# Performance work log

Hardware: AMD Instinct MI355X
Metric: run time of the kernel (lower is better)

## Reference

```python
import jax, jax.numpy as jnp
import numpy as np

B, D, E, H, OUT = 4096, 1024, 8, 4096, 1024


def setup_inputs() -> dict:
    key = jax.random.key(0)
    ks = jax.random.split(key, 8)
    s_in = 1.0 / np.sqrt(D)
    s_h = 1.0 / np.sqrt(H)
    return {
        "x": jax.random.normal(ks[0], (B, D), dtype=jnp.float32),
        "Wg": jax.random.uniform(ks[1], (D, E), minval=-s_in, maxval=s_in, dtype=jnp.float32),
        "bg": jnp.zeros((E,), dtype=jnp.float32),
        "W1": jax.random.uniform(ks[2], (E, D, H), minval=-s_in, maxval=s_in, dtype=jnp.float32),
        "b1": jnp.zeros((E, H), dtype=jnp.float32),
        "W2": jax.random.uniform(ks[3], (E, H, OUT), minval=-s_h, maxval=s_h, dtype=jnp.float32),
        "b2": jnp.zeros((E, OUT), dtype=jnp.float32),
        "w_bal": jnp.float32(0.01),
    }


def reference(x, Wg, bg, W1, b1, W2, b2, w_bal):
    # Gating: softmax then top-1 (== argmax of logits)
    gate_logits = x @ Wg + bg                      # [B, E]
    assign = jnp.argmax(gate_logits, axis=1)       # [B] top-1 expert
    onehot = jax.nn.one_hot(assign, E, dtype=x.dtype)  # [B, E] dispatch mask

    # Dense dispatch: run every expert MLP, combine by one-hot (top-1 select).
    # Original returns raw expert output (no gate-prob scaling).
    h = jax.nn.relu(jnp.einsum("bd,edh->ebh", x, W1) + b1[:, None, :])  # [E, B, H]
    y = jnp.einsum("ebh,eho->ebo", h, W2) + b2[:, None, :]              # [E, B, OUT]
    output = jnp.einsum("ebo,be->bo", y, onehot)                        # [B, OUT]

    # Load-balance loss on per-expert token counts
    loads = onehot.sum(axis=0)                     # [E]
    balance_loss = jnp.sum((loads - loads.mean()) ** 2) / E
    return output, balance_loss * w_bal
```

## Files before the change

kernel.cpp:

```cpp
#include <hip/hip_runtime.h>
#include <hip/hip_bf16.h>

typedef unsigned short u16;
typedef __attribute__((ext_vector_type(8))) short bf16x8;
typedef __attribute__((ext_vector_type(4))) float f32x4;

#define BTOK 4096
#define DDIM 1024
#define NEXP 8
#define HDIM 4096
#define ODIM 1024
#define MAXTILES 40
#define MAXROWS (MAXTILES * 128)

__device__ __forceinline__ u16 f2bf(float f) {
  unsigned u = __float_as_uint(f);
  return (u16)((u + 0x7FFFu + ((u >> 16) & 1u)) >> 16);
}
__device__ __forceinline__ u16 cvt_bf(float f) {
  __hip_bfloat16 h = __float2bfloat16(f);
  u16 r;
  __builtin_memcpy(&r, &h, 2);
  return r;
}

__device__ __forceinline__ void gload16(const void* g, void* l) {
  __builtin_amdgcn_global_load_lds(
      (const __attribute__((address_space(1))) void*)g,
      (__attribute__((address_space(3))) void*)l, 16, 0, 0);
}

__global__ __launch_bounds__(256) void init_kernel(int* __restrict__ ctrl,
                                                   int* __restrict__ rowmap) {
  int i = blockIdx.x * 256 + threadIdx.x;
  if (i < 1024)
    ctrl[i] = 0;
  else
    rowmap[i - 1024] = -1;
}

__global__ __launch_bounds__(256) void gate_kernel(
    const float* __restrict__ x, const float* __restrict__ Wg,
    const float* __restrict__ bg, int* __restrict__ assign,
    int* __restrict__ counts) {
  int wave = threadIdx.x >> 6;
  int lane = threadIdx.x & 63;
  int b = blockIdx.x * 4 + wave;
  const float* xr = x + (size_t)b * DDIM;
  double acc[NEXP];
#pragma unroll
  for (int e = 0; e < NEXP; ++e) acc[e] = 0.0;
  for (int d = lane; d < DDIM; d += 64) {
    float xv = xr[d];
    const float4* wrow = (const float4*)(Wg + d * NEXP);
    float4 w0 = wrow[0], w1 = wrow[1];
    acc[0] += (double)xv * (double)w0.x;
    acc[1] += (double)xv * (double)w0.y;
    acc[2] += (double)xv * (double)w0.z;
    acc[3] += (double)xv * (double)w0.w;
    acc[4] += (double)xv * (double)w1.x;
    acc[5] += (double)xv * (double)w1.y;
    acc[6] += (double)xv * (double)w1.z;
    acc[7] += (double)xv * (double)w1.w;
  }
#pragma unroll
  for (int e = 0; e < NEXP; ++e) {
    double v = acc[e];
#pragma unroll
    for (int off = 32; off > 0; off >>= 1) v += __shfl_xor(v, off);
    acc[e] = v;
  }
  if (lane == 0) {
    int best = 0;
    double bv = acc[0] + (double)bg[0];
#pragma unroll
    for (int e = 1; e < NEXP; ++e) {
      double v = acc[e] + (double)bg[e];
      if (v > bv) { bv = v; best = e; }
    }
    assign[b] = best;
    atomicAdd(&counts[best], 1);
  }
}

__global__ void setup_kernel(const int* __restrict__ counts,
                             const float* __restrict__ wbal,
                             int* __restrict__ offp, int* __restrict__ tile_e,
                             int* __restrict__ tile_m, int* __restrict__ meta,
                             float* __restrict__ loss_out) {
  if (threadIdx.x != 0 || blockIdx.x != 0) return;
  int off = 0, nt = 0;
  for (int e = 0; e < NEXP; ++e) {
    offp[e] = off;
    int pc = (counts[e] + 127) & ~127;
    for (int t = 0; t < (pc >> 7); ++t) {
      tile_e[nt] = e;
      tile_m[nt] = off + t * 128;
      ++nt;
    }
    off += pc;
  }
  offp[NEXP] = off;
  meta[0] = nt;
  float mean = (float)BTOK / (float)NEXP;
  float s = 0.f;
  for (int e = 0; e < NEXP; ++e) {
    float d = (float)counts[e] - mean;
    s += d * d;
  }
  loss_out[0] = s / (float)NEXP * wbal[0];
}

__global__ __launch_bounds__(256) void gather_kernel(
    const float* __restrict__ x, const int* __restrict__ assign,
    const int* __restrict__ offp, int* __restrict__ fill,
    int* __restrict__ rowmap, u16* __restrict__ xg) {
  int b = blockIdx.x;
  __shared__ int srow;
  if (threadIdx.x == 0) {
    int e = assign[b];
    int pos = atomicAdd(&fill[e], 1);
    int row = offp[e] + pos;
    rowmap[row] = b;
    srow = row;
  }
  __syncthreads();
  int row = srow;
  float4 v = *(const float4*)(x + (size_t)b * DDIM + threadIdx.x * 4);
  ushort4 o;
  o.x = f2bf(v.x);
  o.y = f2bf(v.y);
  o.z = f2bf(v.z);
  o.w = f2bf(v.w);
  *(ushort4*)(xg + (size_t)row * DDIM + threadIdx.x * 4) = o;
}

template <int MODE, int LDA, int LDN>
__global__ __launch_bounds__(256, 3) void moe_gemm(
    const u16* __restrict__ A, const float* __restrict__ W, size_t eStride,
    const float* __restrict__ bias, const int* __restrict__ tile_e,
    const int* __restrict__ tile_m, const int* __restrict__ meta,
    u16* __restrict__ Hout, float* __restrict__ P, size_t pStride, int nkt) {
  const int nx = gridDim.x;
  const int nwg = nx * gridDim.y;
  const int orig = blockIdx.y * nx + blockIdx.x;
  const int q = nwg >> 3;
  const int wg = (orig & 7) * q + (orig >> 3);
  const int bx = wg % nx, by = wg / nx;
  if (bx >= meta[0]) return;
  const int e = tile_e[bx];
  const int m0 = tile_m[bx];
  const int n0 = by * 128;
  const int kOff = blockIdx.z * nkt * 32;

  __shared__ __align__(16) u16 lds[2 * 8192];

  const int tid = threadIdx.x;
  const int lane = tid & 63;
  const int wave = tid >> 6;
  const int wr = wave >> 1, wc = wave & 1;
  const int fr = lane & 15;
  const int kqr = lane >> 4;

  const int r0 = tid >> 2, k0 = (tid & 3) ^ ((r0 >> 1) & 3);
  const int r1 = (tid + 256) >> 2, k1 = ((tid + 256) & 3) ^ ((r1 >> 1) & 3);
  const u16* aS0 = A + (size_t)(m0 + r0) * LDA + kOff + k0 * 8;
  const u16* aS1 = A + (size_t)(m0 + r1) * LDA + kOff + k1 * 8;
  const int dst0 = (tid & ~63) * 8;
  const int dst1 = dst0 + 2048;

  const int bc = tid & 127;
  const int bq0 = tid >> 7;
  const float* bRow = W + (size_t)e * eStride + (size_t)kOff * LDN + n0 + bc;
  const int bu0 = (bc * 4 + (bq0 ^ ((bc >> 1) & 3))) * 8;
  const int bu1 = (bc * 4 + ((bq0 + 2) ^ ((bc >> 1) & 3))) * 8;

  int aOff[4], bOff[4];
#pragma unroll
  for (int i = 0; i < 4; ++i) {
    int r = wr * 64 + i * 16 + fr;
    aOff[i] = (r * 4 + (kqr ^ ((r >> 1) & 3))) * 8;
    int c = wc * 64 + i * 16 + fr;
    bOff[i] = (c * 4 + (kqr ^ ((c >> 1) & 3))) * 8;
  }

  f32x4 acc[4][4];
#pragma unroll
  for (int i = 0; i < 4; ++i)
#pragma unroll
    for (int j = 0; j < 4; ++j)
#pragma unroll
      for (int r = 0; r < 4; ++r) acc[i][j][r] = 0.f;

  float fb[16];
  auto loadB = [&](int kt) {
    const float* p = bRow + (size_t)kt * 32 * LDN;
#pragma unroll
    for (int i = 0; i < 8; ++i) fb[i] = p[(size_t)(bq0 * 8 + i) * LDN];
#pragma unroll
    for (int i = 0; i < 8; ++i) fb[8 + i] = p[(size_t)((bq0 + 2) * 8 + i) * LDN];
  };
  auto writeB = [&](int c) {
    u16* ldsB = lds + c * 8192 + 4096;
    alignas(16) u16 tA[8], tB[8];
#pragma unroll
    for (int i = 0; i < 8; ++i) tA[i] = cvt_bf(fb[i]);
#pragma unroll
    for (int i = 0; i < 8; ++i) tB[i] = cvt_bf(fb[8 + i]);
    *(bf16x8*)&ldsB[bu0] = *(const bf16x8*)tA;
    *(bf16x8*)&ldsB[bu1] = *(const bf16x8*)tB;
  };
  auto stageA = [&](int c, int kt) {
    const int ko = kt * 32;
    u16* base = lds + c * 8192;
    gload16(aS0 + ko, base + dst0);
    gload16(aS1 + ko, base + dst1);
  };
  auto compute = [&](int c) {
    const u16* base = lds + c * 8192;
    bf16x8 af[4], bfr[4];
#pragma unroll
    for (int i = 0; i < 4; ++i) {
      af[i] = *(const bf16x8*)(base + aOff[i]);
      bfr[i] = *(const bf16x8*)(base + 4096 + bOff[i]);
    }
#pragma unroll
    for (int i = 0; i < 4; ++i)
#pragma unroll
      for (int j = 0; j < 4; ++j)
        acc[i][j] = __builtin_amdgcn_mfma_f32_16x16x32_bf16(af[i], bfr[j],
                                                            acc[i][j], 0, 0, 0);
  };

  loadB(0);
  stageA(0, 0);
  writeB(0);
  __syncthreads();
  int cur = 0;
#pragma unroll 1
  for (int kt = 0; kt < nkt - 1; ++kt) {
    loadB(kt + 1);
    stageA(cur ^ 1, kt + 1);
    compute(cur);
    writeB(cur ^ 1);
    __syncthreads();
    cur ^= 1;
  }
  compute(cur);

  if constexpr (MODE == 0) {
#pragma unroll
    for (int i = 0; i < 4; ++i) {
      int rbase = m0 + wr * 64 + i * 16 + (lane >> 4) * 4;
#pragma unroll
      for (int j = 0; j < 4; ++j) {
        int col = n0 + wc * 64 + j * 16 + fr;
        float bv = bias[e * LDN + col];
#pragma unroll
        for (int r = 0; r < 4; ++r) {
          float v = acc[i][j][r] + bv;
          v = v > 0.f ? v : 0.f;
          Hout[(size_t)(rbase + r) * LDN + col] = f2bf(v);
        }
      }
    }
  } else {
    float* Pp = P + blockIdx.z * pStride;
#pragma unroll
    for (int i = 0; i < 4; ++i) {
      int rbase = m0 + wr * 64 + i * 16 + (lane >> 4) * 4;
#pragma unroll
      for (int j = 0; j < 4; ++j) {
        int col = n0 + wc * 64 + j * 16 + fr;
#pragma unroll
        for (int r = 0; r < 4; ++r)
          Pp[(size_t)(rbase + r) * ODIM + col] = acc[i][j][r];
      }
    }
  }
}

__global__ __launch_bounds__(256) void reduce_kernel(
    const float* __restrict__ P, size_t pStride, const int* __restrict__ rowmap,
    const int* __restrict__ tile_e, const int* __restrict__ tile_m,
    const int* __restrict__ meta, const float* __restrict__ b2,
    float* __restrict__ out) {
  if ((int)blockIdx.x >= meta[0]) return;
  const int e = tile_e[blockIdx.x];
  const int m0 = tile_m[blockIdx.x];
  const int c0 = blockIdx.y * 128;
#pragma unroll 1
  for (int it = 0; it < 16; ++it) {
    int idx = it * 256 + threadIdx.x;
    int r = idx >> 5, cq = idx & 31;
    int row = m0 + r;
    int tok = rowmap[row];
    if (tok < 0) continue;
    int c = c0 + cq * 4;
    float4 a = *(const float4*)(P + (size_t)row * ODIM + c);
    float4 b = *(const float4*)(P + pStride + (size_t)row * ODIM + c);
    float4 bb = *(const float4*)(b2 + (size_t)e * ODIM + c);
    float4 o;
    o.x = a.x + b.x + bb.x;
    o.y = a.y + b.y + bb.y;
    o.z = a.z + b.z + bb.z;
    o.w = a.w + b.w + bb.w;
    *(float4*)(out + (size_t)tok * ODIM + c) = o;
  }
}

extern "C" void kernel_launch(void* const* d_in, const int* in_sizes, int n_in,
                              void* d_out, int out_size, void* d_ws,
                              size_t ws_size, hipStream_t stream) {
  const float* x = (const float*)d_in[0];
  const float* Wg = (const float*)d_in[1];
  const float* bg = (const float*)d_in[2];
  const float* W1 = (const float*)d_in[3];
  const float* b1 = (const float*)d_in[4];
  const float* W2 = (const float*)d_in[5];
  const float* b2 = (const float*)d_in[6];
  const float* wbal = (const float*)d_in[7];
  float* out = (float*)d_out;

  char* ws = (char*)d_ws;
  int* counts = (int*)(ws + 0);
  int* fill = (int*)(ws + 64);
  int* offp = (int*)(ws + 128);
  int* meta = (int*)(ws + 192);
  int* tile_e = (int*)(ws + 256);
  int* tile_m = (int*)(ws + 512);
  int* assign = (int*)(ws + 4096);
  int* rowmap = (int*)(ws + 20480);
  u16* xg = (u16*)(ws + 65536);
  u16* h = (u16*)(ws + 10551296);
  float* P = (float*)(ws + 52494336);
  const size_t pStride = (size_t)MAXROWS * ODIM;

  init_kernel<<<24, 256, 0, stream>>>((int*)ws, rowmap);
  gate_kernel<<<BTOK / 4, 256, 0, stream>>>(x, Wg, bg, assign, counts);
  setup_kernel<<<1, 64, 0, stream>>>(counts, wbal, offp, tile_e, tile_m, meta,
                                     out + (size_t)BTOK * ODIM);
  gather_kernel<<<BTOK, 256, 0, stream>>>(x, assign, offp, fill, rowmap, xg);

  moe_gemm<0, DDIM, HDIM><<<dim3(MAXTILES, HDIM / 128, 1), 256, 0, stream>>>(
      xg, W1, (size_t)DDIM * HDIM, b1, tile_e, tile_m, meta, h, nullptr, 0,
      DDIM / 32);
  moe_gemm<1, HDIM, ODIM><<<dim3(MAXTILES, ODIM / 128, 2), 256, 0, stream>>>(
      h, W2, (size_t)HDIM * ODIM, nullptr, tile_e, tile_m, meta, nullptr, P,
      pStride, HDIM / 64);

  reduce_kernel<<<dim3(MAXTILES, ODIM / 128), 256, 0, stream>>>(
      P, pStride, rowmap, tile_e, tile_m, meta, b2, out);
}
```

Before: 327.8 us.

## Deepen MoE GEMM pipeline with triple-buffered A and two-ahead B prefetch

```diff
diff --git a/kernel.cpp b/kernel.cpp
--- a/kernel.cpp
+++ b/kernel.cpp
@@ -153,7 +153,8 @@
   const int n0 = by * 128;
   const int kOff = blockIdx.z * nkt * 32;
 
-  __shared__ __align__(16) u16 lds[2 * 8192];
+  __shared__ __align__(16) u16 Alds[3 * 4096];
+  __shared__ __align__(16) u16 Blds[2 * 4096];
 
   const int tid = threadIdx.x;
   const int lane = tid & 63;
@@ -192,37 +193,39 @@
 #pragma unroll
       for (int r = 0; r < 4; ++r) acc[i][j][r] = 0.f;
 
-  float fb[16];
-  auto loadB = [&](int kt) {
+  float fb0[16], fb1[16];
+
+  auto stageA = [&](int buf, int kt) {
+    const int ko = kt * 32;
+    u16* base = Alds + buf * 4096;
+    gload16(aS0 + ko, base + dst0);
+    gload16(aS1 + ko, base + dst1);
+  };
+  auto loadB = [&](float (&f)[16], int kt) {
     const float* p = bRow + (size_t)kt * 32 * LDN;
 #pragma unroll
-    for (int i = 0; i < 8; ++i) fb[i] = p[(size_t)(bq0 * 8 + i) * LDN];
-#pragma unroll
-    for (int i = 0; i < 8; ++i) fb[8 + i] = p[(size_t)((bq0 + 2) * 8 + i) * LDN];
+    for (int i = 0; i < 8; ++i) f[i] = p[(size_t)(bq0 * 8 + i) * LDN];
+#pragma unroll
+    for (int i = 0; i < 8; ++i) f[8 + i] = p[(size_t)((bq0 + 2) * 8 + i) * LDN];
   };
-  auto writeB = [&](int c) {
-    u16* ldsB = lds + c * 8192 + 4096;
+  auto writeB = [&](const float (&f)[16], int buf) {
+    u16* ldsB = Blds + buf * 4096;
     alignas(16) u16 tA[8], tB[8];
 #pragma unroll
-    for (int i = 0; i < 8; ++i) tA[i] = cvt_bf(fb[i]);
-#pragma unroll
-    for (int i = 0; i < 8; ++i) tB[i] = cvt_bf(fb[8 + i]);
+    for (int i = 0; i < 8; ++i) tA[i] = cvt_bf(f[i]);
+#pragma unroll
+    for (int i = 0; i < 8; ++i) tB[i] = cvt_bf(f[8 + i]);
     *(bf16x8*)&ldsB[bu0] = *(const bf16x8*)tA;
     *(bf16x8*)&ldsB[bu1] = *(const bf16x8*)tB;
   };
-  auto stageA = [&](int c, int kt) {
-    const int ko = kt * 32;
-    u16* base = lds + c * 8192;
-    gload16(aS0 + ko, base + dst0);
-    gload16(aS1 + ko, base + dst1);
-  };
-  auto compute = [&](int c) {
-    const u16* base = lds + c * 8192;
+  auto compute = [&](int abuf, int bbuf) {
+    const u16* aB = Alds + abuf * 4096;
+    const u16* bB = Blds + bbuf * 4096;
     bf16x8 af[4], bfr[4];
 #pragma unroll
     for (int i = 0; i < 4; ++i) {
-      af[i] = *(const bf16x8*)(base + aOff[i]);
-      bfr[i] = *(const bf16x8*)(base + 4096 + bOff[i]);
+      af[i] = *(const bf16x8*)(aB + aOff[i]);
+      bfr[i] = *(const bf16x8*)(bB + bOff[i]);
     }
 #pragma unroll
     for (int i = 0; i < 4; ++i)
@@ -232,21 +235,42 @@
                                                             acc[i][j], 0, 0, 0);
   };
 
-  loadB(0);
+#define BAR()                                              \
+  asm volatile("s_waitcnt lgkmcnt(0)" ::: "memory");       \
+  __builtin_amdgcn_sched_barrier(0);                       \
+  __builtin_amdgcn_s_barrier();                            \
+  __builtin_amdgcn_sched_barrier(0);
+
+#define STEP(T, FC, FN)                                    \
+  {                                                        \
+    if ((T) + 2 < nkt) {                                   \
+      stageA(sa, (T) + 2);                                 \
+      sa = (sa == 2) ? 0 : sa + 1;                         \
+      loadB(FN, (T) + 2);                                  \
+    }                                                      \
+    compute(ca, (T) & 1);                                  \
+    ca = (ca == 2) ? 0 : ca + 1;                           \
+    writeB(FC, ((T) + 1) & 1);                             \
+    BAR();                                                 \
+  }
+
   stageA(0, 0);
-  writeB(0);
-  __syncthreads();
-  int cur = 0;
+  stageA(1, 1);
+  loadB(fb0, 0);
+  writeB(fb0, 0);
+  loadB(fb0, 1);
+  BAR();
+
+  int ca = 0, sa = 2;
+  STEP(0, fb0, fb1);
 #pragma unroll 1
-  for (int kt = 0; kt < nkt - 1; ++kt) {
-    loadB(kt + 1);
-    stageA(cur ^ 1, kt + 1);
-    compute(cur);
-    writeB(cur ^ 1);
-    __syncthreads();
-    cur ^= 1;
-  }
-  compute(cur);
+  for (int t = 1; t + 1 < nkt; t += 2) {
+    STEP(t, fb1, fb0);
+    STEP(t + 1, fb0, fb1);
+  }
+  compute(ca, (nkt - 1) & 1);
+#undef STEP
+#undef BAR
 
   if constexpr (MODE == 0) {
 #pragma unroll
```

Result: no change. 328.0 us (+0.1%).

## Pre-transpose weights to bf16 and drop split-K with fused scatter epilogue

Applied to the files above, without the earlier changes.

```diff
diff --git a/kernel.cpp b/kernel.cpp
--- a/kernel.cpp
+++ b/kernel.cpp
@@ -135,25 +135,40 @@
   *(ushort4*)(xg + (size_t)row * DDIM + threadIdx.x * 4) = o;
 }
 
-template <int MODE, int LDA, int LDN>
-__global__ __launch_bounds__(256, 3) void moe_gemm(
-    const u16* __restrict__ A, const float* __restrict__ W, size_t eStride,
+__global__ __launch_bounds__(256) void transpose_conv(
+    const float* __restrict__ W, u16* __restrict__ wt, int N, int K) {
+  const int e = blockIdx.z;
+  const int kb = blockIdx.x * 256, nb = blockIdx.y * 64;
+  __shared__ __align__(16) float lds[256][66];
+  const float* src = W + (size_t)e * K * N;
+  const int t = threadIdx.x;
+  const int rr = t >> 4, cc = (t & 15) * 4;
+#pragma unroll
+  for (int p = 0; p < 16; ++p) {
+    float4 v =
+        *(const float4*)(src + (size_t)(kb + rr + p * 16) * N + nb + cc);
+    *(float4*)&lds[rr + p * 16][cc] = v;
+  }
+  __syncthreads();
+  const int n = t & 63, kg = (t >> 6) * 64;
+  alignas(16) u16 tmp[64];
+#pragma unroll
+  for (int i = 0; i < 64; ++i) tmp[i] = cvt_bf(lds[kg + i][n]);
+  u16* dst = wt + ((size_t)e * N + nb + n) * K + kb + kg;
+#pragma unroll
+  for (int q = 0; q < 8; ++q) *(float4*)(dst + q * 8) = *(float4*)&tmp[q * 8];
+}
+
+template <int MODE>
+__device__ __forceinline__ void gemm_core(
+    u16* lds, int bx, int by, const u16* __restrict__ A, int lda,
+    const u16* __restrict__ BT, int ldb, int nbRows,
     const float* __restrict__ bias, const int* __restrict__ tile_e,
-    const int* __restrict__ tile_m, const int* __restrict__ meta,
-    u16* __restrict__ Hout, float* __restrict__ P, size_t pStride, int nkt) {
-  const int nx = gridDim.x;
-  const int nwg = nx * gridDim.y;
-  const int orig = blockIdx.y * nx + blockIdx.x;
-  const int q = nwg >> 3;
-  const int wg = (orig & 7) * q + (orig >> 3);
-  const int bx = wg % nx, by = wg / nx;
-  if (bx >= meta[0]) return;
+    const int* __restrict__ tile_m, const int* __restrict__ rowmap,
+    u16* __restrict__ Hout, int ldn, float* __restrict__ Cout, int nkt) {
   const int e = tile_e[bx];
   const int m0 = tile_m[bx];
   const int n0 = by * 128;
-  const int kOff = blockIdx.z * nkt * 32;
-
-  __shared__ __align__(16) u16 lds[2 * 8192];
 
   const int tid = threadIdx.x;
   const int lane = tid & 63;
@@ -164,16 +179,13 @@
 
   const int r0 = tid >> 2, k0 = (tid & 3) ^ ((r0 >> 1) & 3);
   const int r1 = (tid + 256) >> 2, k1 = ((tid + 256) & 3) ^ ((r1 >> 1) & 3);
-  const u16* aS0 = A + (size_t)(m0 + r0) * LDA + kOff + k0 * 8;
-  const u16* aS1 = A + (size_t)(m0 + r1) * LDA + kOff + k1 * 8;
+  const u16* aS0 = A + (size_t)(m0 + r0) * lda + k0 * 8;
+  const u16* aS1 = A + (size_t)(m0 + r1) * lda + k1 * 8;
+  const u16* bPan = BT + ((size_t)e * nbRows + n0) * ldb;
+  const u16* bS0 = bPan + (size_t)r0 * ldb + k0 * 8;
+  const u16* bS1 = bPan + (size_t)r1 * ldb + k1 * 8;
   const int dst0 = (tid & ~63) * 8;
   const int dst1 = dst0 + 2048;
-
-  const int bc = tid & 127;
-  const int bq0 = tid >> 7;
-  const float* bRow = W + (size_t)e * eStride + (size_t)kOff * LDN + n0 + bc;
-  const int bu0 = (bc * 4 + (bq0 ^ ((bc >> 1) & 3))) * 8;
-  const int bu1 = (bc * 4 + ((bq0 + 2) ^ ((bc >> 1) & 3))) * 8;
 
   int aOff[4], bOff[4];
 #pragma unroll
@@ -192,29 +204,13 @@
 #pragma unroll
       for (int r = 0; r < 4; ++r) acc[i][j][r] = 0.f;
 
-  float fb[16];
-  auto loadB = [&](int kt) {
-    const float* p = bRow + (size_t)kt * 32 * LDN;
-#pragma unroll
-    for (int i = 0; i < 8; ++i) fb[i] = p[(size_t)(bq0 * 8 + i) * LDN];
-#pragma unroll
-    for (int i = 0; i < 8; ++i) fb[8 + i] = p[(size_t)((bq0 + 2) * 8 + i) * LDN];
-  };
-  auto writeB = [&](int c) {
-    u16* ldsB = lds + c * 8192 + 4096;
-    alignas(16) u16 tA[8], tB[8];
-#pragma unroll
-    for (int i = 0; i < 8; ++i) tA[i] = cvt_bf(fb[i]);
-#pragma unroll
-    for (int i = 0; i < 8; ++i) tB[i] = cvt_bf(fb[8 + i]);
-    *(bf16x8*)&ldsB[bu0] = *(const bf16x8*)tA;
-    *(bf16x8*)&ldsB[bu1] = *(const bf16x8*)tB;
-  };
-  auto stageA = [&](int c, int kt) {
+  auto stage = [&](int c, int kt) {
     const int ko = kt * 32;
     u16* base = lds + c * 8192;
     gload16(aS0 + ko, base + dst0);
     gload16(aS1 + ko, base + dst1);
+    gload16(bS0 + ko, base + 4096 + dst0);
+    gload16(bS1 + ko, base + 4096 + dst1);
   };
   auto compute = [&](int c) {
     const u16* base = lds + c * 8192;
@@ -232,17 +228,13 @@
                                                             acc[i][j], 0, 0, 0);
   };
 
-  loadB(0);
-  stageA(0, 0);
-  writeB(0);
+  stage(0, 0);
   __syncthreads();
   int cur = 0;
 #pragma unroll 1
   for (int kt = 0; kt < nkt - 1; ++kt) {
-    loadB(kt + 1);
-    stageA(cur ^ 1, kt + 1);
+    stage(cur ^ 1, kt + 1);
     compute(cur);
-    writeB(cur ^ 1);
     __syncthreads();
     cur ^= 1;
   }
@@ -255,58 +247,62 @@
 #pragma unroll
       for (int j = 0; j < 4; ++j) {
         int col = n0 + wc * 64 + j * 16 + fr;
-        float bv = bias[e * LDN + col];
+        float bv = bias[e * ldn + col];
 #pragma unroll
         for (int r = 0; r < 4; ++r) {
           float v = acc[i][j][r] + bv;
           v = v > 0.f ? v : 0.f;
-          Hout[(size_t)(rbase + r) * LDN + col] = f2bf(v);
+          Hout[(size_t)(rbase + r) * ldn + col] = f2bf(v);
         }
       }
     }
   } else {
-    float* Pp = P + blockIdx.z * pStride;
 #pragma unroll
     for (int i = 0; i < 4; ++i) {
       int rbase = m0 + wr * 64 + i * 16 + (lane >> 4) * 4;
+      int tok[4];
+#pragma unroll
+      for (int r = 0; r < 4; ++r) tok[r] = rowmap[rbase + r];
 #pragma unroll
       for (int j = 0; j < 4; ++j) {
         int col = n0 + wc * 64 + j * 16 + fr;
-#pragma unroll
-        for (int r = 0; r < 4; ++r)
-          Pp[(size_t)(rbase + r) * ODIM + col] = acc[i][j][r];
+        float bv = bias[e * ldn + col];
+#pragma unroll
+        for (int r = 0; r < 4; ++r) {
+          if (tok[r] >= 0)
+            Cout[(size_t)tok[r] * ODIM + col] = acc[i][j][r] + bv;
+        }
       }
     }
   }
 }
 
-__global__ __launch_bounds__(256) void reduce_kernel(
-    const float* __restrict__ P, size_t pStride, const int* __restrict__ rowmap,
-    const int* __restrict__ tile_e, const int* __restrict__ tile_m,
-    const int* __restrict__ meta, const float* __restrict__ b2,
-    float* __restrict__ out) {
-  if ((int)blockIdx.x >= meta[0]) return;
-  const int e = tile_e[blockIdx.x];
-  const int m0 = tile_m[blockIdx.x];
-  const int c0 = blockIdx.y * 128;
-#pragma unroll 1
-  for (int it = 0; it < 16; ++it) {
-    int idx = it * 256 + threadIdx.x;
-    int r = idx >> 5, cq = idx & 31;
-    int row = m0 + r;
-    int tok = rowmap[row];
-    if (tok < 0) continue;
-    int c = c0 + cq * 4;
-    float4 a = *(const float4*)(P + (size_t)row * ODIM + c);
-    float4 b = *(const float4*)(P + pStride + (size_t)row * ODIM + c);
-    float4 bb = *(const float4*)(b2 + (size_t)e * ODIM + c);
-    float4 o;
-    o.x = a.x + b.x + bb.x;
-    o.y = a.y + b.y + bb.y;
-    o.z = a.z + b.z + bb.z;
-    o.w = a.w + b.w + bb.w;
-    *(float4*)(out + (size_t)tok * ODIM + c) = o;
-  }
+__global__ __launch_bounds__(256) void moe_gemm1(
+    const u16* __restrict__ xg, const u16* __restrict__ wt1,
+    const float* __restrict__ b1, const int* __restrict__ tile_e,
+    const int* __restrict__ tile_m, const int* __restrict__ meta,
+    u16* __restrict__ h) {
+  __shared__ __align__(16) u16 lds[2 * 8192];
+  const int orig = blockIdx.y * MAXTILES + blockIdx.x;
+  const int wg = (orig & 7) * 160 + (orig >> 3);
+  const int bx = wg % MAXTILES, by = wg / MAXTILES;
+  if (bx >= meta[0]) return;
+  gemm_core<0>(lds, bx, by, xg, DDIM, wt1, DDIM, HDIM, b1, tile_e, tile_m,
+               nullptr, h, HDIM, nullptr, DDIM / 32);
+}
+
+__global__ __launch_bounds__(256) void moe_gemm2(
+    const u16* __restrict__ h, const u16* __restrict__ wt2,
+    const float* __restrict__ b2, const int* __restrict__ tile_e,
+    const int* __restrict__ tile_m, const int* __restrict__ meta,
+    const int* __restrict__ rowmap, float* __restrict__ out) {
+  __shared__ __align__(16) u16 lds[2 * 8192];
+  const int orig = blockIdx.y * MAXTILES + blockIdx.x;
+  const int wg = (orig & 7) * 40 + (orig >> 3);
+  const int bx = wg % MAXTILES, by = wg / MAXTILES;
+  if (bx >= meta[0]) return;
+  gemm_core<1>(lds, bx, by, h, HDIM, wt2, HDIM, ODIM, b2, tile_e, tile_m,
+               rowmap, nullptr, ODIM, out, HDIM / 32);
 }
 
 extern "C" void kernel_launch(void* const* d_in, const int* in_sizes, int n_in,
@@ -333,8 +329,8 @@
   int* rowmap = (int*)(ws + 20480);
   u16* xg = (u16*)(ws + 65536);
   u16* h = (u16*)(ws + 10551296);
-  float* P = (float*)(ws + 52494336);
-  const size_t pStride = (size_t)MAXROWS * ODIM;
+  u16* wt1 = (u16*)(ws + 52494336);
+  u16* wt2 = (u16*)(ws + 119603200);
 
   init_kernel<<<24, 256, 0, stream>>>((int*)ws, rowmap);
   gate_kernel<<<BTOK / 4, 256, 0, stream>>>(x, Wg, bg, assign, counts);
@@ -342,13 +338,13 @@
                                      out + (size_t)BTOK * ODIM);
   gather_kernel<<<BTOK, 256, 0, stream>>>(x, assign, offp, fill, rowmap, xg);
 
-  moe_gemm<0, DDIM, HDIM><<<dim3(MAXTILES, HDIM / 128, 1), 256, 0, stream>>>(
-      xg, W1, (size_t)DDIM * HDIM, b1, tile_e, tile_m, meta, h, nullptr, 0,
-      DDIM / 32);
-  moe_gemm<1, HDIM, ODIM><<<dim3(MAXTILES, ODIM / 128, 2), 256, 0, stream>>>(
-      h, W2, (size_t)HDIM * ODIM, nullptr, tile_e, tile_m, meta, nullptr, P,
-      pStride, HDIM / 64);
-
-  reduce_kernel<<<dim3(MAXTILES, ODIM / 128), 256, 0, stream>>>(
-      P, pStride, rowmap, tile_e, tile_m, meta, b2, out);
-}
+  transpose_conv<<<dim3(DDIM / 256, HDIM / 64, NEXP), 256, 0, stream>>>(
+      W1, wt1, HDIM, DDIM);
+  transpose_conv<<<dim3(HDIM / 256, ODIM / 64, NEXP), 256, 0, stream>>>(
+      W2, wt2, ODIM, HDIM);
+
+  moe_gemm1<<<dim3(MAXTILES, HDIM / 128), 256, 0, stream>>>(
+      xg, wt1, b1, tile_e, tile_m, meta, h);
+  moe_gemm2<<<dim3(MAXTILES, ODIM / 128), 256, 0, stream>>>(
+      h, wt2, b2, tile_e, tile_m, meta, rowmap, out);
+}
```

Result: slower. 363.1 us (+10.8%).
